# Optimization experiments

Measured on AMD Instinct MI355X. Metric: run time of the kernel, lower is better.

## Reference

```python
import jax, jax.numpy as jnp
import numpy as np

OBS_LEN = 16          # observation_len in SnapKV
KERNEL = 5            # AvgPool1d kernel_size
MAX_CACHE_LEN = 2048  # max_cache_length


def _avg_pool1d_nopad(x, k=KERNEL):
    """AvgPool1d(kernel=k, stride=1, padding=k//2, count_include_pad=False) over last axis."""
    S = x.shape[-1]
    pad = k // 2
    zero = jnp.zeros(x.shape[:-1] + (1,), x.dtype)
    c0 = jnp.concatenate([zero, jnp.cumsum(x, axis=-1)], axis=-1)  # [..., S+1]
    i = jnp.arange(S)
    hi = jnp.minimum(i + pad + 1, S)  # exclusive window end
    lo = jnp.maximum(i - pad, 0)      # inclusive window start
    wsum = jnp.take(c0, hi, axis=-1) - jnp.take(c0, lo, axis=-1)
    return wsum / (hi - lo).astype(x.dtype)


def setup_inputs() -> dict:
    key = jax.random.key(0)
    k1, k2, k3 = jax.random.split(key, 3)
    B, H, Q, S, D = 1, 32, 64, 8192, 128
    # realistic attention weights: softmax over key axis
    attn = jax.nn.softmax(jax.random.normal(k1, (B, H, Q, S), jnp.float32), axis=-1)
    k_val = jax.random.normal(k2, (B, H, S, D), jnp.float32)
    v_val = jax.random.normal(k3, (B, H, S, D), jnp.float32)
    input_pos = jnp.arange(S, dtype=jnp.int32)
    return {"attn": attn, "k_val": k_val, "v_val": v_val, "input_pos": input_pos}


def reference(attn, k_val, v_val, input_pos):
    # ---- SnapKV prompt compression (_compress_prompt_w_snapkv) ----
    # priority: mean attention received by each key over the last OBS_LEN queries
    priority = attn[:, :, -OBS_LEN:, :].mean(axis=2)          # [B, H, S]
    attn_history = priority                                    # pre-pooling copy
    pooled = _avg_pool1d_nopad(priority)                       # [B, H, S]
    pooled = pooled.at[:, :, -OBS_LEN:].set(1.0)               # always keep observation window
    _, keep_idxs = jax.lax.top_k(pooled, MAX_CACHE_LEN)        # [B, H, L]
    keep_idxs = jnp.sort(keep_idxs, axis=-1)
    attn_history_c = jnp.take_along_axis(attn_history, keep_idxs, axis=-1)  # [B, H, L]
    idx4 = keep_idxs[..., None]                                # [B, H, L, 1]
    k_compressed = jnp.take_along_axis(k_val, idx4, axis=2)    # [B, H, L, D]
    v_compressed = jnp.take_along_axis(v_val, idx4, axis=2)    # [B, H, L, D]
    # ---- cache fill (update / fill_headwise): compressed tokens fill the whole cache ----
    k_cache = k_compressed
    v_cache = v_compressed
    pos = keep_idxs[0].astype(jnp.int32)                       # head-specific positions, [H, L]
    return k_cache, v_cache, attn_history_c, pos
```

## Files before the change

kernel.cpp:

```cpp
#include <hip/hip_runtime.h>

#define H 32
#define Q 64
#define S 8192
#define D 128
#define OBS 16
#define L 2048

typedef float f32x4 __attribute__((ext_vector_type(4)));

__global__ __launch_bounds__(1024) void k_priosel(
    const float* __restrict__ attn,
    int* __restrict__ keep,
    float* __restrict__ hist_out)
{
    __shared__ float pr[S];
    __shared__ int whist[4][16][257];
    __shared__ int wtot[16];
    __shared__ int res_byte, res_k;

    const int h = blockIdx.x;
    const int tid = threadIdx.x;
    const int lane = tid & 63, wid = tid >> 6;

    for (int i = tid; i < 4 * 16 * 257; i += 1024) ((int*)whist)[i] = 0;

    {
        const float* abase = attn + (size_t)(h * Q + (Q - OBS)) * S;
        f32x4 a00 = {0.f, 0.f, 0.f, 0.f}, a01 = a00, a10 = a00, a11 = a00;
#pragma unroll
        for (int q = 0; q < OBS; q += 2) {
            const f32x4* r0 = (const f32x4*)(abase + (size_t)q * S);
            const f32x4* r1 = (const f32x4*)(abase + (size_t)(q + 1) * S);
            a00 += __builtin_nontemporal_load(r0 + tid);
            a01 += __builtin_nontemporal_load(r0 + tid + 1024);
            a10 += __builtin_nontemporal_load(r1 + tid);
            a11 += __builtin_nontemporal_load(r1 + tid + 1024);
        }
        const float inv = 1.0f / (float)OBS;
        ((f32x4*)pr)[tid] = (a00 + a10) * inv;
        ((f32x4*)pr)[tid + 1024] = (a01 + a11) * inv;
    }
    __syncthreads();

    unsigned key[8];
    const int s0 = tid * 8;
    {
        float w[12];
#pragma unroll
        for (int i = 0; i < 12; ++i) {
            int idx = s0 - 2 + i;
            w[i] = (idx >= 0 && idx < S) ? pr[idx] : 0.f;
        }
#pragma unroll
        for (int j = 0; j < 8; ++j) {
            int s = s0 + j;
            float pooled;
            if (s >= S - OBS) {
                pooled = 1.0f;
            } else {
                int lo = s - 2; if (lo < 0) lo = 0;
                int hi = s + 3;
                float sum = 0.f;
                for (int i = lo; i < hi; ++i) sum += w[i - s0 + 2];
                pooled = sum / (float)(hi - lo);
            }
            key[j] = __float_as_uint(pooled);
        }
    }

    unsigned prefix = 0;
    int k = L;
    for (int pass = 3; pass >= 0; --pass) {
        const int shift = pass * 8;
        {
            int cur = -1, run = 0;
#pragma unroll
            for (int j = 0; j < 8; ++j) {
                unsigned kk = key[j];
                bool match = (pass == 3) || ((kk >> (shift + 8)) == prefix);
                int b = match ? (int)((kk >> shift) & 255u) : -1;
                if (b != cur) {
                    if (cur >= 0) atomicAdd(&whist[pass][wid][cur], run);
                    cur = b; run = 1;
                } else {
                    run++;
                }
            }
            if (cur >= 0) atomicAdd(&whist[pass][wid][cur], run);
        }
        __syncthreads();
        if (wid == 0) {
            int b0 = 0, b1 = 0, b2 = 0, b3 = 0;
            const int bb0 = 4 * lane;
#pragma unroll
            for (int w = 0; w < 16; ++w) {
                b0 += whist[pass][w][bb0 + 0];
                b1 += whist[pass][w][bb0 + 1];
                b2 += whist[pass][w][bb0 + 2];
                b3 += whist[pass][w][bb0 + 3];
            }
            int lane_sum = b0 + b1 + b2 + b3;
            int suffix = lane_sum;
#pragma unroll
            for (int off = 1; off < 64; off <<= 1) {
                int u = __shfl_down(suffix, off);
                if (lane + off < 64) suffix += u;
            }
            int suffix_next = suffix - lane_sum;
            if (suffix >= k && suffix_next < k) {
                int bins[4] = {b0, b1, b2, b3};
                int cum = suffix_next;
                for (int bb = 3; bb >= 0; --bb) {
                    int nc = cum + bins[bb];
                    if (nc >= k) { res_byte = bb0 + bb; res_k = k - cum; break; }
                    cum = nc;
                }
            }
        }
        __syncthreads();
        prefix = (prefix << 8) | (unsigned)res_byte;
        k = res_k;
    }
    const unsigned T = prefix;
    const int needed_eq = k;

    int gt = 0, eq = 0;
#pragma unroll
    for (int j = 0; j < 8; ++j) {
        gt += (key[j] > T) ? 1 : 0;
        eq += (key[j] == T) ? 1 : 0;
    }
    int packed = (gt << 16) | eq;
    int v = packed;
#pragma unroll
    for (int off = 1; off < 64; off <<= 1) {
        int u = __shfl_up(v, off);
        if (lane >= off) v += u;
    }
    if (lane == 63) wtot[wid] = v;
    __syncthreads();
    int base = 0;
    for (int w = 0; w < wid; ++w) base += wtot[w];
    int excl = base + v - packed;
    int gt_before = excl >> 16;
    int eq_before = excl & 0xffff;

    {
        int g = gt_before, e = eq_before;
#pragma unroll
        for (int j = 0; j < 8; ++j) {
            bool isgt = key[j] > T;
            bool iseq = key[j] == T;
            bool sel = isgt || (iseq && (e < needed_eq));
            if (sel) {
                int s = s0 + j;
                int rank = g + (e < needed_eq ? e : needed_eq);
                size_t o = (size_t)h * L + rank;
                keep[o] = s;
                hist_out[o] = pr[s];
            }
            g += isgt ? 1 : 0;
            e += iseq ? 1 : 0;
        }
    }
}

__global__ void k_gather(const float* __restrict__ kv_k, const float* __restrict__ kv_v,
                         const int* __restrict__ keep, float* __restrict__ out,
                         float* __restrict__ pos_out) {
    const int tid = threadIdx.x;
    const int l32 = tid & 31;
    const int i0 = (blockIdx.x * 8 + (tid >> 5)) * 4;
    const int h = i0 >> 11;
    const int4 kk = *(const int4*)(keep + i0);
    const int sI[4] = {kk.x, kk.y, kk.z, kk.w};
    if (l32 < 4) pos_out[i0 + l32] = (float)sI[l32];
#pragma unroll
    for (int t = 0; t < 4; ++t) {
        const int idx = i0 + t;
        const f32x4* srcK = (const f32x4*)(kv_k + (size_t)(h * S + sI[t]) * D);
        const f32x4* srcV = (const f32x4*)(kv_v + (size_t)(h * S + sI[t]) * D);
        f32x4* dstK = (f32x4*)(out + (size_t)idx * D);
        f32x4* dstV = (f32x4*)(out + ((size_t)H * L + idx) * D);
        __builtin_nontemporal_store(__builtin_nontemporal_load(srcK + l32), dstK + l32);
        __builtin_nontemporal_store(__builtin_nontemporal_load(srcV + l32), dstV + l32);
    }
}

extern "C" void kernel_launch(void* const* d_in, const int* in_sizes, int n_in,
                              void* d_out, int out_size, void* d_ws, size_t ws_size,
                              hipStream_t stream) {
    const float* attn = (const float*)d_in[0];
    const float* k_val = (const float*)d_in[1];
    const float* v_val = (const float*)d_in[2];

    float* out = (float*)d_out;
    float* hist = out + (size_t)2 * H * L * D;
    float* pos = hist + (size_t)H * L;

    int* keep = (int*)d_ws;

    k_priosel<<<H, 1024, 0, stream>>>(attn, keep, hist);
    k_gather<<<(H * L) / 32, 256, 0, stream>>>(k_val, v_val, keep, out, pos);
}
```

Measured before the change: 289.3 us.

## Split priority reduction into a separate widely parallel kernel before selection

```diff
diff --git a/kernel.cpp b/kernel.cpp
--- a/kernel.cpp
+++ b/kernel.cpp
@@ -9,8 +9,26 @@
 
 typedef float f32x4 __attribute__((ext_vector_type(4)));
 
-__global__ __launch_bounds__(1024) void k_priosel(
-    const float* __restrict__ attn,
+__global__ void k_priority(const float* __restrict__ attn, float* __restrict__ prio) {
+    const int gid = blockIdx.x;
+    const int h = gid >> 3;
+    const int chunk = gid & 7;
+    const int s4 = chunk * 1024 + threadIdx.x * 4;
+    const f32x4* base = (const f32x4*)(attn + ((size_t)(h * Q + (Q - OBS)) * S + s4));
+    f32x4 a0 = {0.f, 0.f, 0.f, 0.f}, a1 = a0, a2 = a0, a3 = a0;
+#pragma unroll
+    for (int q = 0; q < OBS; q += 4) {
+        a0 += __builtin_nontemporal_load(base + (size_t)(q + 0) * (S / 4));
+        a1 += __builtin_nontemporal_load(base + (size_t)(q + 1) * (S / 4));
+        a2 += __builtin_nontemporal_load(base + (size_t)(q + 2) * (S / 4));
+        a3 += __builtin_nontemporal_load(base + (size_t)(q + 3) * (S / 4));
+    }
+    const f32x4 r = (a0 + a1 + a2 + a3) * (1.0f / (float)OBS);
+    *((f32x4*)(prio + (size_t)h * S + s4)) = r;
+}
+
+__global__ __launch_bounds__(1024) void k_select(
+    const float* __restrict__ prio,
     int* __restrict__ keep,
     float* __restrict__ hist_out)
 {
@@ -23,23 +41,11 @@
     const int tid = threadIdx.x;
     const int lane = tid & 63, wid = tid >> 6;
 
-    for (int i = tid; i < 4 * 16 * 257; i += 1024) ((int*)whist)[i] = 0;
-
     {
-        const float* abase = attn + (size_t)(h * Q + (Q - OBS)) * S;
-        f32x4 a00 = {0.f, 0.f, 0.f, 0.f}, a01 = a00, a10 = a00, a11 = a00;
-#pragma unroll
-        for (int q = 0; q < OBS; q += 2) {
-            const f32x4* r0 = (const f32x4*)(abase + (size_t)q * S);
-            const f32x4* r1 = (const f32x4*)(abase + (size_t)(q + 1) * S);
-            a00 += __builtin_nontemporal_load(r0 + tid);
-            a01 += __builtin_nontemporal_load(r0 + tid + 1024);
-            a10 += __builtin_nontemporal_load(r1 + tid);
-            a11 += __builtin_nontemporal_load(r1 + tid + 1024);
-        }
-        const float inv = 1.0f / (float)OBS;
-        ((f32x4*)pr)[tid] = (a00 + a10) * inv;
-        ((f32x4*)pr)[tid + 1024] = (a01 + a11) * inv;
+        const f32x4* src = (const f32x4*)(prio + (size_t)h * S);
+        ((f32x4*)pr)[tid] = src[tid];
+        ((f32x4*)pr)[tid + 1024] = src[tid + 1024];
+        for (int i = tid; i < 4 * 16 * 257; i += 1024) ((int*)whist)[i] = 0;
     }
     __syncthreads();
 
@@ -199,8 +205,10 @@
     float* hist = out + (size_t)2 * H * L * D;
     float* pos = hist + (size_t)H * L;
 
-    int* keep = (int*)d_ws;
-
-    k_priosel<<<H, 1024, 0, stream>>>(attn, keep, hist);
+    float* prio = (float*)d_ws;
+    int* keep = (int*)((char*)d_ws + (size_t)H * S * sizeof(float));
+
+    k_priority<<<256, 256, 0, stream>>>(attn, prio);
+    k_select<<<H, 1024, 0, stream>>>(prio, keep, hist);
     k_gather<<<(H * L) / 32, 256, 0, stream>>>(k_val, v_val, keep, out, pos);
 }
```

New measurement: 286.3 us. About the same (-1.1%).
